# Kernel optimization log

Hardware: AMD Instinct MI355X
Metric: run time of the kernel (lower is better)

## Reference

```python
import jax, jax.numpy as jnp
import numpy as np

B, K, F, E = 32, 1024, 128, 128  # batch, window_size(num_nodes), n_features, embed_dim
OUT2 = 125                       # lin2 output dim (hardcoded in module)
ALPHA = 0.2                      # LeakyReLU negative slope


def setup_inputs() -> dict:
    key = jax.random.key(0)
    ks = jax.random.split(key, 7)
    x = jax.random.normal(ks[0], (B, K, F), dtype=jnp.float32)
    lin_w = jax.random.normal(ks[1], (E, F), dtype=jnp.float32) * 0.05
    lin_b = jax.random.normal(ks[2], (E,), dtype=jnp.float32) * 0.01
    a = jax.random.normal(ks[3], (2 * E, 1), dtype=jnp.float32) * 0.1  # xavier-ish
    bias = jax.random.normal(ks[4], (K, K), dtype=jnp.float32) * 0.02
    lin2_w = jax.random.normal(ks[5], (OUT2, K), dtype=jnp.float32) * 0.03
    lin2_b = jax.random.normal(ks[6], (OUT2,), dtype=jnp.float32) * 0.01
    return {"x": x, "lin_w": lin_w, "lin_b": lin_b, "a": a, "bias": bias,
            "lin2_w": lin2_w, "lin2_b": lin2_b}


def reference(x, lin_w, lin_b, a, bias, lin2_w, lin2_b):
    # Wx = lin(x): [B,K,E]
    Wx = jnp.einsum('bkf,ef->bke', x, lin_w) + lin_b
    # Additive attention scores. Original concatenates (Wx_i, Wx_j) -> [B,K,K,2E]
    # then matmuls with a [2E,1]. Identity: concat @ a == Wx_i@a1 + Wx_j@a2.
    a1 = a[:E, 0]   # [E]
    a2 = a[E:, 0]   # [E]
    s1 = Wx @ a1    # [B,K]  (row/query term, from repeat_interleave)
    s2 = Wx @ a2    # [B,K]  (col/key term, from repeat)
    e = jax.nn.leaky_relu(s1[:, :, None] + s2[:, None, :], negative_slope=ALPHA)
    e = e + bias                              # [B,K,K]
    attention = jax.nn.softmax(e, axis=2)     # softmax over last dim (keys)
    h = jnp.einsum('bij,bjf->bif', attention, x) + x   # [B,K,F], residual
    # permute(0,2,1) -> [B,F,K]; lin2 contracts K -> 125
    h2 = jnp.einsum('bkf,ok->bfo', h, lin2_w) + lin2_b  # [B,F,125]
    h2 = jax.nn.relu(h2)
    return (h2, attention)
```

## Files before the change

### kernel.cpp

```cpp
#include <hip/hip_runtime.h>

#define B_ 32
#define K_ 1024
#define F_ 128
#define E_ 128
#define OUT2_ 125
#define ALPHA_ 0.2f

typedef __bf16 bf16x8_t __attribute__((ext_vector_type(8)));
typedef float  f32x4_t  __attribute__((ext_vector_type(4)));

__device__ __forceinline__ unsigned short f2bf(float f) {
    unsigned u = __float_as_uint(f);
    u = (u + 0x7fffu + ((u >> 16) & 1u)) >> 16;
    return (unsigned short)u;
}

__global__ void k_prep(const float* __restrict__ lin_w, const float* __restrict__ lin_b,
                       const float* __restrict__ a, float* __restrict__ ws) {
    int t = threadIdx.x;
    if (t < 128) {
        float acc = 0.f;
        for (int e = 0; e < E_; ++e) acc += lin_w[e * F_ + t] * a[e];
        ws[t] = acc;
    } else {
        int f = t - 128;
        float acc = 0.f;
        for (int e = 0; e < E_; ++e) acc += lin_w[e * F_ + f] * a[E_ + e];
        ws[128 + f] = acc;
    }
    if (t == 0) { float c = 0.f; for (int e = 0; e < E_; ++e) c += lin_b[e] * a[e];       ws[256] = c; }
    if (t == 1) { float c = 0.f; for (int e = 0; e < E_; ++e) c += lin_b[e] * a[E_ + e];  ws[257] = c; }
}

__global__ __launch_bounds__(256) void k_scores(const float* __restrict__ x,
                                                const float* __restrict__ ws,
                                                float* __restrict__ s1, float* __restrict__ s2) {
    int wave = threadIdx.x >> 6;
    int lane = threadIdx.x & 63;
    int row = blockIdx.x * 4 + wave;
    const float* xr = x + (size_t)row * F_;
    float x0 = xr[lane], x1 = xr[lane + 64];
    float p1 = x0 * ws[lane]       + x1 * ws[lane + 64];
    float p2 = x0 * ws[128 + lane] + x1 * ws[192 + lane];
    for (int m = 32; m; m >>= 1) { p1 += __shfl_xor(p1, m, 64); p2 += __shfl_xor(p2, m, 64); }
    if (lane == 0) { s1[row] = p1 + ws[256]; s2[row] = p2 + ws[257]; }
}

__global__ __launch_bounds__(256) void k_xt(const float* __restrict__ x,
                                            unsigned short* __restrict__ xt) {
    int kt = blockIdx.x;
    int b  = blockIdx.y;
    int t  = threadIdx.x;
    __shared__ float xs[64 * 132];
    const float* xb = x + ((size_t)b * K_ + kt * 64) * F_;
#pragma unroll
    for (int q = 0; q < 8; ++q) {
        int flat = q * 256 + t;
        int kk = flat >> 5, f4 = flat & 31;
        float4 v = *(const float4*)(xb + (size_t)kk * F_ + f4 * 4);
        xs[kk * 132 + f4 * 4]     = v.x;
        xs[kk * 132 + f4 * 4 + 1] = v.y;
        xs[kk * 132 + f4 * 4 + 2] = v.z;
        xs[kk * 132 + f4 * 4 + 3] = v.w;
    }
    __syncthreads();
    int f = t >> 1, half = t & 1;
    union { unsigned short u[32]; uint4 v[4]; } pack;
#pragma unroll
    for (int i = 0; i < 32; ++i) pack.u[i] = f2bf(xs[(half * 32 + i) * 132 + f]);
    unsigned short* dst = xt + (((size_t)(b * 16 + kt) * 128 + f) * 64 + half * 32);
    uint4* d4 = (uint4*)dst;
#pragma unroll
    for (int i = 0; i < 4; ++i) d4[i] = pack.v[i];
}

__global__ __launch_bounds__(256) void k_softmax(const float* __restrict__ s1,
                                                 const float* __restrict__ s2,
                                                 const float* __restrict__ bias,
                                                 float* __restrict__ att) {
    int i = blockIdx.x >> 5;
    int b = blockIdx.x & 31;
    int t = threadIdx.x;
    float sv = s1[b * K_ + i];
    float4 s2v = ((const float4*)(s2 + b * K_))[t];
    float4 bv  = ((const float4*)(bias + (size_t)i * K_))[t];
    float e[4];
    {
        float v;
        v = sv + s2v.x; v = v > 0.f ? v : ALPHA_ * v; e[0] = __expf(v + bv.x);
        v = sv + s2v.y; v = v > 0.f ? v : ALPHA_ * v; e[1] = __expf(v + bv.y);
        v = sv + s2v.z; v = v > 0.f ? v : ALPHA_ * v; e[2] = __expf(v + bv.z);
        v = sv + s2v.w; v = v > 0.f ? v : ALPHA_ * v; e[3] = __expf(v + bv.w);
    }
    float sum = e[0] + e[1] + e[2] + e[3];
    for (int m = 32; m; m >>= 1) sum += __shfl_xor(sum, m, 64);
    __shared__ float reds[4];
    int wave = t >> 6, lane = t & 63;
    if (lane == 0) reds[wave] = sum;
    __syncthreads();
    sum = reds[0] + reds[1] + reds[2] + reds[3];
    float r = 1.f / sum;
    float4 o; o.x = e[0] * r; o.y = e[1] * r; o.z = e[2] * r; o.w = e[3] * r;
    ((float4*)(att + ((size_t)b * K_ + i) * K_))[t] = o;
}

__global__ __launch_bounds__(256) void k_attx(const float* __restrict__ att,
                                              const unsigned short* __restrict__ xt,
                                              const float* __restrict__ x,
                                              unsigned short* __restrict__ h) {
    int b  = blockIdx.y;
    int i0 = blockIdx.x * 64;
    int t  = threadIdx.x;
    int wave = t >> 6, lane = t & 63;
    int quad = lane >> 4, l15 = lane & 15;

    __shared__ unsigned short A_s[64 * 72];
    __shared__ unsigned short X_s[128 * 72];

    const float* ab = att + ((size_t)b * K_ + i0) * K_;

    f32x4_t acc[4][2];
#pragma unroll
    for (int m = 0; m < 4; ++m)
#pragma unroll
        for (int n = 0; n < 2; ++n) acc[m][n] = (f32x4_t)(0.f);

    int ai = t >> 2, aq = t & 3;
    int xf = t >> 1, xh = t & 1;

    for (int kt = 0; kt < 16; ++kt) {
        int k0 = kt * 64;
        __syncthreads();
        {
            const float* src = ab + (size_t)ai * K_ + k0 + aq * 16;
            union { unsigned short u[16]; uint4 v[2]; } p;
#pragma unroll
            for (int q = 0; q < 4; ++q) {
                float4 v = *(const float4*)(src + q * 4);
                p.u[q * 4]     = f2bf(v.x);
                p.u[q * 4 + 1] = f2bf(v.y);
                p.u[q * 4 + 2] = f2bf(v.z);
                p.u[q * 4 + 3] = f2bf(v.w);
            }
            uint4* d = (uint4*)&A_s[ai * 72 + aq * 16];
            d[0] = p.v[0]; d[1] = p.v[1];
        }
        {
            const uint4* src = (const uint4*)(xt + ((size_t)(b * 16 + kt)) * 128 * 64) + t * 4;
            uint4* d = (uint4*)&X_s[xf * 72 + xh * 32];
#pragma unroll
            for (int q = 0; q < 4; ++q) d[q] = src[q];
        }
        __syncthreads();
#pragma unroll
        for (int kh = 0; kh < 2; ++kh) {
            bf16x8_t af[4], bff[2];
#pragma unroll
            for (int m = 0; m < 4; ++m)
                af[m] = *(const bf16x8_t*)&A_s[(m * 16 + l15) * 72 + kh * 32 + quad * 8];
#pragma unroll
            for (int n = 0; n < 2; ++n)
                bff[n] = *(const bf16x8_t*)&X_s[(wave * 32 + n * 16 + l15) * 72 + kh * 32 + quad * 8];
#pragma unroll
            for (int m = 0; m < 4; ++m)
#pragma unroll
                for (int n = 0; n < 2; ++n)
                    acc[m][n] = __builtin_amdgcn_mfma_f32_16x16x32_bf16(af[m], bff[n], acc[m][n], 0, 0, 0);
        }
    }
#pragma unroll
    for (int m = 0; m < 4; ++m) {
#pragma unroll
        for (int n = 0; n < 2; ++n) {
            int f = wave * 32 + n * 16 + l15;
#pragma unroll
            for (int r = 0; r < 4; ++r) {
                int i = i0 + m * 16 + quad * 4 + r;
                size_t idx = ((size_t)b * K_ + i) * F_ + f;
                h[idx] = f2bf(acc[m][n][r] + x[idx]);
            }
        }
    }
}

__global__ __launch_bounds__(256) void k_out2p(const unsigned short* __restrict__ h,
                                               const float* __restrict__ w2,
                                               float* __restrict__ part) {
    int b  = blockIdx.y;
    int f0 = blockIdx.x * 16;
    int ks = blockIdx.z;
    int t = threadIdx.x;
    int o = t & 127;
    int g = t >> 7;
    __shared__ float hs[32 * 24];
    __shared__ float wt[128 * 33];
    const unsigned short* hb = h + (size_t)b * K_ * F_;
    float acc[8];
#pragma unroll
    for (int r = 0; r < 8; ++r) acc[r] = 0.f;

    int kbeg = ks * 256, kend = kbeg + 256;
    for (int k0 = kbeg; k0 < kend; k0 += 32) {
        {
            int idx = t * 2;
            int kk = idx >> 4, ff = idx & 15;
            unsigned pair = *(const unsigned*)(hb + (size_t)(k0 + kk) * F_ + f0 + ff);
            hs[kk * 24 + ff]     = __uint_as_float((pair & 0xFFFFu) << 16);
            hs[kk * 24 + ff + 1] = __uint_as_float((pair >> 16) << 16);
        }
#pragma unroll
        for (int q = 0; q < 16; ++q) {
            int idx = q * 256 + t;
            int oo = idx >> 5, kk = idx & 31;
            wt[oo * 33 + kk] = (oo < OUT2_) ? w2[(size_t)oo * K_ + k0 + kk] : 0.f;
        }
        __syncthreads();
#pragma unroll 8
        for (int kk = 0; kk < 32; ++kk) {
            float4 h0 = *(const float4*)&hs[kk * 24 + g * 8];
            float4 h1 = *(const float4*)&hs[kk * 24 + g * 8 + 4];
            float wv = wt[o * 33 + kk];
            acc[0] += h0.x * wv; acc[1] += h0.y * wv;
            acc[2] += h0.z * wv; acc[3] += h0.w * wv;
            acc[4] += h1.x * wv; acc[5] += h1.y * wv;
            acc[6] += h1.z * wv; acc[7] += h1.w * wv;
        }
        __syncthreads();
    }
#pragma unroll
    for (int r = 0; r < 8; ++r) {
        int f = f0 + g * 8 + r;
        part[((size_t)(ks * 32 + b) * 128 + f) * 128 + o] = acc[r];
    }
}

__global__ __launch_bounds__(256) void k_out2e(const float* __restrict__ part,
                                               const float* __restrict__ b2,
                                               float* __restrict__ out) {
    int idx = blockIdx.x * 256 + threadIdx.x;
    if (idx >= B_ * F_ * OUT2_) return;
    int o  = idx % OUT2_;
    int bf = idx / OUT2_;
    float v = b2[o];
#pragma unroll
    for (int s = 0; s < 4; ++s) v += part[((size_t)s * 4096 + bf) * 128 + o];
    out[idx] = v > 0.f ? v : 0.f;
}

extern "C" void kernel_launch(void* const* d_in, const int* in_sizes, int n_in,
                              void* d_out, int out_size, void* d_ws, size_t ws_size,
                              hipStream_t stream) {
    const float* x      = (const float*)d_in[0];
    const float* lin_w  = (const float*)d_in[1];
    const float* lin_b  = (const float*)d_in[2];
    const float* a      = (const float*)d_in[3];
    const float* bias   = (const float*)d_in[4];
    const float* lin2_w = (const float*)d_in[5];
    const float* lin2_b = (const float*)d_in[6];

    float* out = (float*)d_out;
    float* h2  = out;
    float* att = out + (size_t)B_ * F_ * OUT2_;

    float* ws = (float*)d_ws;
    float* s1 = ws + 512;
    float* s2 = ws + 512 + B_ * K_;
    unsigned short* h  = (unsigned short*)(ws + 512 + 2 * B_ * K_);
    unsigned short* xt = h + (size_t)B_ * K_ * F_;
    float* part = (float*)xt;

    k_prep<<<1, 256, 0, stream>>>(lin_w, lin_b, a, ws);
    k_scores<<<(B_ * K_) / 4, 256, 0, stream>>>(x, ws, s1, s2);
    k_xt<<<dim3(16, B_), 256, 0, stream>>>(x, xt);
    k_softmax<<<B_ * K_, 256, 0, stream>>>(s1, s2, bias, att);
    k_attx<<<dim3(K_ / 64, B_), 256, 0, stream>>>(att, xt, x, h);
    k_out2p<<<dim3(F_ / 16, B_, 4), 256, 0, stream>>>(h, lin2_w, part);
    k_out2e<<<(B_ * F_ * OUT2_ + 255) / 256, 256, 0, stream>>>(part, lin2_b, h2);
}
```

Before: 308.6 us.

## Fuse softmax into attention-times-x kernel, recomputing exps instead of rereading attention

The separate softmax kernel is removed. The attention GEMM kernel now first computes each row's exp-sum from s1, s2 and bias. It then recomputes the normalized probabilities inside the K loop, writes them to the output with nontemporal stores, and feeds them as bf16 to the MFMA. This drops the 128MB round trip of reading attention back from memory. In exchange, every exp is computed twice, and the GEMM kernel takes on extra ALU work and bias reads.

```diff
diff --git a/kernel.cpp b/kernel.cpp
--- a/kernel.cpp
+++ b/kernel.cpp
@@ -75,39 +75,12 @@
     for (int i = 0; i < 4; ++i) d4[i] = pack.v[i];
 }
 
-__global__ __launch_bounds__(256) void k_softmax(const float* __restrict__ s1,
-                                                 const float* __restrict__ s2,
-                                                 const float* __restrict__ bias,
-                                                 float* __restrict__ att) {
-    int i = blockIdx.x >> 5;
-    int b = blockIdx.x & 31;
-    int t = threadIdx.x;
-    float sv = s1[b * K_ + i];
-    float4 s2v = ((const float4*)(s2 + b * K_))[t];
-    float4 bv  = ((const float4*)(bias + (size_t)i * K_))[t];
-    float e[4];
-    {
-        float v;
-        v = sv + s2v.x; v = v > 0.f ? v : ALPHA_ * v; e[0] = __expf(v + bv.x);
-        v = sv + s2v.y; v = v > 0.f ? v : ALPHA_ * v; e[1] = __expf(v + bv.y);
-        v = sv + s2v.z; v = v > 0.f ? v : ALPHA_ * v; e[2] = __expf(v + bv.z);
-        v = sv + s2v.w; v = v > 0.f ? v : ALPHA_ * v; e[3] = __expf(v + bv.w);
-    }
-    float sum = e[0] + e[1] + e[2] + e[3];
-    for (int m = 32; m; m >>= 1) sum += __shfl_xor(sum, m, 64);
-    __shared__ float reds[4];
-    int wave = t >> 6, lane = t & 63;
-    if (lane == 0) reds[wave] = sum;
-    __syncthreads();
-    sum = reds[0] + reds[1] + reds[2] + reds[3];
-    float r = 1.f / sum;
-    float4 o; o.x = e[0] * r; o.y = e[1] * r; o.z = e[2] * r; o.w = e[3] * r;
-    ((float4*)(att + ((size_t)b * K_ + i) * K_))[t] = o;
-}
-
-__global__ __launch_bounds__(256) void k_attx(const float* __restrict__ att,
+__global__ __launch_bounds__(256) void k_attx(const float* __restrict__ s1,
+                                              const float* __restrict__ s2,
+                                              const float* __restrict__ bias,
                                               const unsigned short* __restrict__ xt,
                                               const float* __restrict__ x,
+                                              float* __restrict__ att,
                                               unsigned short* __restrict__ h) {
     int b  = blockIdx.y;
     int i0 = blockIdx.x * 64;
@@ -117,8 +90,27 @@
 
     __shared__ unsigned short A_s[64 * 72];
     __shared__ unsigned short X_s[128 * 72];
-
-    const float* ab = att + ((size_t)b * K_ + i0) * K_;
+    __shared__ float rvs[64];
+
+    int ai = t >> 2, aq = t & 3;
+    float sv = s1[b * K_ + i0 + ai];
+
+    const float4* s2r = (const float4*)(s2 + (size_t)b * K_);
+    const float4* br  = (const float4*)(bias + (size_t)(i0 + ai) * K_);
+    float sum = 0.f;
+#pragma unroll 4
+    for (int q = 0; q < 64; ++q) {
+        float4 s2v = s2r[q * 4 + aq];
+        float4 bv  = br[q * 4 + aq];
+        float v;
+        v = sv + s2v.x; v = v > 0.f ? v : ALPHA_ * v; sum += __expf(v + bv.x);
+        v = sv + s2v.y; v = v > 0.f ? v : ALPHA_ * v; sum += __expf(v + bv.y);
+        v = sv + s2v.z; v = v > 0.f ? v : ALPHA_ * v; sum += __expf(v + bv.z);
+        v = sv + s2v.w; v = v > 0.f ? v : ALPHA_ * v; sum += __expf(v + bv.w);
+    }
+    sum += __shfl_xor(sum, 1, 64);
+    sum += __shfl_xor(sum, 2, 64);
+    if (aq == 0) rvs[ai] = 1.f / sum;
 
     f32x4_t acc[4][2];
 #pragma unroll
@@ -126,22 +118,33 @@
 #pragma unroll
         for (int n = 0; n < 2; ++n) acc[m][n] = (f32x4_t)(0.f);
 
-    int ai = t >> 2, aq = t & 3;
     int xf = t >> 1, xh = t & 1;
 
     for (int kt = 0; kt < 16; ++kt) {
         int k0 = kt * 64;
         __syncthreads();
         {
-            const float* src = ab + (size_t)ai * K_ + k0 + aq * 16;
+            int kb = k0 + aq * 16;
+            float rv = rvs[ai];
+            const float4* s2p = (const float4*)(s2 + (size_t)b * K_ + kb);
+            const float4* bp  = (const float4*)(bias + (size_t)(i0 + ai) * K_ + kb);
+            f32x4_t* ap = (f32x4_t*)(att + ((size_t)b * K_ + i0 + ai) * K_ + kb);
             union { unsigned short u[16]; uint4 v[2]; } p;
 #pragma unroll
             for (int q = 0; q < 4; ++q) {
-                float4 v = *(const float4*)(src + q * 4);
-                p.u[q * 4]     = f2bf(v.x);
-                p.u[q * 4 + 1] = f2bf(v.y);
-                p.u[q * 4 + 2] = f2bf(v.z);
-                p.u[q * 4 + 3] = f2bf(v.w);
+                float4 s2v = s2p[q];
+                float4 bv  = bp[q];
+                f32x4_t e;
+                float v;
+                v = sv + s2v.x; v = v > 0.f ? v : ALPHA_ * v; e[0] = __expf(v + bv.x) * rv;
+                v = sv + s2v.y; v = v > 0.f ? v : ALPHA_ * v; e[1] = __expf(v + bv.y) * rv;
+                v = sv + s2v.z; v = v > 0.f ? v : ALPHA_ * v; e[2] = __expf(v + bv.z) * rv;
+                v = sv + s2v.w; v = v > 0.f ? v : ALPHA_ * v; e[3] = __expf(v + bv.w) * rv;
+                __builtin_nontemporal_store(e, ap + q);
+                p.u[q * 4]     = f2bf(e[0]);
+                p.u[q * 4 + 1] = f2bf(e[1]);
+                p.u[q * 4 + 2] = f2bf(e[2]);
+                p.u[q * 4 + 3] = f2bf(e[3]);
             }
             uint4* d = (uint4*)&A_s[ai * 72 + aq * 16];
             d[0] = p.v[0]; d[1] = p.v[1];
@@ -273,8 +276,7 @@
     k_prep<<<1, 256, 0, stream>>>(lin_w, lin_b, a, ws);
     k_scores<<<(B_ * K_) / 4, 256, 0, stream>>>(x, ws, s1, s2);
     k_xt<<<dim3(16, B_), 256, 0, stream>>>(x, xt);
-    k_softmax<<<B_ * K_, 256, 0, stream>>>(s1, s2, bias, att);
-    k_attx<<<dim3(K_ / 64, B_), 256, 0, stream>>>(att, xt, x, h);
+    k_attx<<<dim3(K_ / 64, B_), 256, 0, stream>>>(s1, s2, bias, xt, x, att, h);
     k_out2p<<<dim3(F_ / 16, B_, 4), 256, 0, stream>>>(h, lin2_w, part);
     k_out2e<<<(B_ * F_ * OUT2_ + 255) / 256, 256, 0, stream>>>(part, lin2_b, h2);
 }
```

Result: slower. 478.2 us (+55.0%).

## Recompute attention probabilities in attx from scores instead of reading att

Applied to the files above, without the earlier changes.

The attention-times-x kernel no longer reads the 128MB fp32 attention matrix written by the softmax kernel. It rebuilds each softmax row from s1, s2 and bias, first with a row-sum pass and then by recomputing the exponentials per tile. This removes a large read of HBM traffic in exchange for extra exp work and a second read of the bias rows, which are small and shared across batches and so likely cache-resident. The softmax kernel still writes att because it is an output.

```diff
diff --git a/kernel.cpp b/kernel.cpp
--- a/kernel.cpp
+++ b/kernel.cpp
@@ -105,7 +105,9 @@
     ((float4*)(att + ((size_t)b * K_ + i) * K_))[t] = o;
 }
 
-__global__ __launch_bounds__(256) void k_attx(const float* __restrict__ att,
+__global__ __launch_bounds__(256) void k_attx(const float* __restrict__ s1,
+                                              const float* __restrict__ s2,
+                                              const float* __restrict__ bias,
                                               const unsigned short* __restrict__ xt,
                                               const float* __restrict__ x,
                                               unsigned short* __restrict__ h) {
@@ -117,8 +119,29 @@
 
     __shared__ unsigned short A_s[64 * 72];
     __shared__ unsigned short X_s[128 * 72];
-
-    const float* ab = att + ((size_t)b * K_ + i0) * K_;
+    __shared__ float rvs[64];
+
+    int ai = t >> 2, aq = t & 3;
+    float sv = s1[b * K_ + i0 + ai];
+
+    const float4* s2r = (const float4*)(s2 + (size_t)b * K_);
+    const float4* br  = (const float4*)(bias + (size_t)(i0 + ai) * K_);
+    float sum = 0.f;
+#pragma unroll 4
+    for (int q = 0; q < 64; ++q) {
+        float4 s2v = s2r[q * 4 + aq];
+        float4 bv  = br[q * 4 + aq];
+        float v;
+        v = sv + s2v.x; v = v > 0.f ? v : ALPHA_ * v; sum += __expf(v + bv.x);
+        v = sv + s2v.y; v = v > 0.f ? v : ALPHA_ * v; sum += __expf(v + bv.y);
+        v = sv + s2v.z; v = v > 0.f ? v : ALPHA_ * v; sum += __expf(v + bv.z);
+        v = sv + s2v.w; v = v > 0.f ? v : ALPHA_ * v; sum += __expf(v + bv.w);
+    }
+    sum += __shfl_xor(sum, 1, 64);
+    sum += __shfl_xor(sum, 2, 64);
+    if (aq == 0) rvs[ai] = 1.f / sum;
+    __syncthreads();
+    float rv = rvs[ai];
 
     f32x4_t acc[4][2];
 #pragma unroll
@@ -126,22 +149,25 @@
 #pragma unroll
         for (int n = 0; n < 2; ++n) acc[m][n] = (f32x4_t)(0.f);
 
-    int ai = t >> 2, aq = t & 3;
     int xf = t >> 1, xh = t & 1;
 
     for (int kt = 0; kt < 16; ++kt) {
         int k0 = kt * 64;
         __syncthreads();
         {
-            const float* src = ab + (size_t)ai * K_ + k0 + aq * 16;
+            int kb = k0 + aq * 16;
+            const float4* s2p = (const float4*)(s2 + (size_t)b * K_ + kb);
+            const float4* bp  = (const float4*)(bias + (size_t)(i0 + ai) * K_ + kb);
             union { unsigned short u[16]; uint4 v[2]; } p;
 #pragma unroll
             for (int q = 0; q < 4; ++q) {
-                float4 v = *(const float4*)(src + q * 4);
-                p.u[q * 4]     = f2bf(v.x);
-                p.u[q * 4 + 1] = f2bf(v.y);
-                p.u[q * 4 + 2] = f2bf(v.z);
-                p.u[q * 4 + 3] = f2bf(v.w);
+                float4 s2v = s2p[q];
+                float4 bv  = bp[q];
+                float v, e;
+                v = sv + s2v.x; v = v > 0.f ? v : ALPHA_ * v; e = __expf(v + bv.x) * rv; p.u[q * 4]     = f2bf(e);
+                v = sv + s2v.y; v = v > 0.f ? v : ALPHA_ * v; e = __expf(v + bv.y) * rv; p.u[q * 4 + 1] = f2bf(e);
+                v = sv + s2v.z; v = v > 0.f ? v : ALPHA_ * v; e = __expf(v + bv.z) * rv; p.u[q * 4 + 2] = f2bf(e);
+                v = sv + s2v.w; v = v > 0.f ? v : ALPHA_ * v; e = __expf(v + bv.w) * rv; p.u[q * 4 + 3] = f2bf(e);
             }
             uint4* d = (uint4*)&A_s[ai * 72 + aq * 16];
             d[0] = p.v[0]; d[1] = p.v[1];
@@ -274,7 +300,7 @@
     k_scores<<<(B_ * K_) / 4, 256, 0, stream>>>(x, ws, s1, s2);
     k_xt<<<dim3(16, B_), 256, 0, stream>>>(x, xt);
     k_softmax<<<B_ * K_, 256, 0, stream>>>(s1, s2, bias, att);
-    k_attx<<<dim3(K_ / 64, B_), 256, 0, stream>>>(att, xt, x, h);
+    k_attx<<<dim3(K_ / 64, B_), 256, 0, stream>>>(s1, s2, bias, xt, x, h);
     k_out2p<<<dim3(F_ / 16, B_, 4), 256, 0, stream>>>(h, lin2_w, part);
     k_out2e<<<(B_ * F_ * OUT2_ + 255) / 256, 256, 0, stream>>>(part, lin2_b, h2);
 }
```

Measured after the change: 330.7 us. +7.1%, slower.

## Use MFMA for lin2 with transposed h and halve attx row tile

Applied to the files above, without the earlier changes.

The attention-times-x kernel now writes h transposed ([B,F,K]) and uses 32-row tiles, doubling its grid. The scalar FP32 lin2 split-K kernel and its reduction kernel are replaced by one bf16 MFMA kernel that converts lin2_w to bf16 in shared memory and fuses bias and ReLU. This removes the partial-sum buffer, one launch and the scalar FMA loop. The cost is lower precision for lin2 weights, only 64 blocks in the new kernel, and lin2_w re-converted by every block.

```diff
diff --git a/kernel.cpp b/kernel.cpp
--- a/kernel.cpp
+++ b/kernel.cpp
@@ -108,43 +108,38 @@
 __global__ __launch_bounds__(256) void k_attx(const float* __restrict__ att,
                                               const unsigned short* __restrict__ xt,
                                               const float* __restrict__ x,
-                                              unsigned short* __restrict__ h) {
+                                              unsigned short* __restrict__ ht) {
     int b  = blockIdx.y;
-    int i0 = blockIdx.x * 64;
+    int i0 = blockIdx.x * 32;
     int t  = threadIdx.x;
     int wave = t >> 6, lane = t & 63;
     int quad = lane >> 4, l15 = lane & 15;
 
-    __shared__ unsigned short A_s[64 * 72];
+    __shared__ unsigned short A_s[32 * 72];
     __shared__ unsigned short X_s[128 * 72];
 
     const float* ab = att + ((size_t)b * K_ + i0) * K_;
 
-    f32x4_t acc[4][2];
-#pragma unroll
-    for (int m = 0; m < 4; ++m)
+    f32x4_t acc[2][2];
+#pragma unroll
+    for (int m = 0; m < 2; ++m)
 #pragma unroll
         for (int n = 0; n < 2; ++n) acc[m][n] = (f32x4_t)(0.f);
 
-    int ai = t >> 2, aq = t & 3;
+    int ai = t >> 3, aq = t & 7;
     int xf = t >> 1, xh = t & 1;
 
     for (int kt = 0; kt < 16; ++kt) {
         int k0 = kt * 64;
         __syncthreads();
         {
-            const float* src = ab + (size_t)ai * K_ + k0 + aq * 16;
-            union { unsigned short u[16]; uint4 v[2]; } p;
-#pragma unroll
-            for (int q = 0; q < 4; ++q) {
-                float4 v = *(const float4*)(src + q * 4);
-                p.u[q * 4]     = f2bf(v.x);
-                p.u[q * 4 + 1] = f2bf(v.y);
-                p.u[q * 4 + 2] = f2bf(v.z);
-                p.u[q * 4 + 3] = f2bf(v.w);
-            }
-            uint4* d = (uint4*)&A_s[ai * 72 + aq * 16];
-            d[0] = p.v[0]; d[1] = p.v[1];
+            const float* src = ab + (size_t)ai * K_ + k0 + aq * 8;
+            float4 v0 = *(const float4*)(src);
+            float4 v1 = *(const float4*)(src + 4);
+            union { unsigned short u[8]; uint4 v; } p;
+            p.u[0] = f2bf(v0.x); p.u[1] = f2bf(v0.y); p.u[2] = f2bf(v0.z); p.u[3] = f2bf(v0.w);
+            p.u[4] = f2bf(v1.x); p.u[5] = f2bf(v1.y); p.u[6] = f2bf(v1.z); p.u[7] = f2bf(v1.w);
+            *(uint4*)&A_s[ai * 72 + aq * 8] = p.v;
         }
         {
             const uint4* src = (const uint4*)(xt + ((size_t)(b * 16 + kt)) * 128 * 64) + t * 4;
@@ -155,97 +150,110 @@
         __syncthreads();
 #pragma unroll
         for (int kh = 0; kh < 2; ++kh) {
-            bf16x8_t af[4], bff[2];
-#pragma unroll
-            for (int m = 0; m < 4; ++m)
+            bf16x8_t af[2], bff[2];
+#pragma unroll
+            for (int m = 0; m < 2; ++m)
                 af[m] = *(const bf16x8_t*)&A_s[(m * 16 + l15) * 72 + kh * 32 + quad * 8];
 #pragma unroll
             for (int n = 0; n < 2; ++n)
                 bff[n] = *(const bf16x8_t*)&X_s[(wave * 32 + n * 16 + l15) * 72 + kh * 32 + quad * 8];
 #pragma unroll
-            for (int m = 0; m < 4; ++m)
+            for (int m = 0; m < 2; ++m)
 #pragma unroll
                 for (int n = 0; n < 2; ++n)
                     acc[m][n] = __builtin_amdgcn_mfma_f32_16x16x32_bf16(af[m], bff[n], acc[m][n], 0, 0, 0);
         }
     }
 #pragma unroll
-    for (int m = 0; m < 4; ++m) {
+    for (int m = 0; m < 2; ++m) {
 #pragma unroll
         for (int n = 0; n < 2; ++n) {
             int f = wave * 32 + n * 16 + l15;
+            int ib = i0 + m * 16 + quad * 4;
+            union { unsigned short u[4]; ushort4 v; } p;
 #pragma unroll
             for (int r = 0; r < 4; ++r) {
-                int i = i0 + m * 16 + quad * 4 + r;
-                size_t idx = ((size_t)b * K_ + i) * F_ + f;
-                h[idx] = f2bf(acc[m][n][r] + x[idx]);
-            }
-        }
-    }
-}
-
-__global__ __launch_bounds__(256) void k_out2p(const unsigned short* __restrict__ h,
+                int i = ib + r;
+                p.u[r] = f2bf(acc[m][n][r] + x[((size_t)b * K_ + i) * F_ + f]);
+            }
+            *(ushort4*)&ht[((size_t)b * F_ + f) * K_ + ib] = p.v;
+        }
+    }
+}
+
+__global__ __launch_bounds__(256) void k_out2m(const unsigned short* __restrict__ ht,
                                                const float* __restrict__ w2,
-                                               float* __restrict__ part) {
-    int b  = blockIdx.y;
-    int f0 = blockIdx.x * 16;
-    int ks = blockIdx.z;
-    int t = threadIdx.x;
-    int o = t & 127;
-    int g = t >> 7;
-    __shared__ float hs[32 * 24];
-    __shared__ float wt[128 * 33];
-    const unsigned short* hb = h + (size_t)b * K_ * F_;
-    float acc[8];
-#pragma unroll
-    for (int r = 0; r < 8; ++r) acc[r] = 0.f;
-
-    int kbeg = ks * 256, kend = kbeg + 256;
-    for (int k0 = kbeg; k0 < kend; k0 += 32) {
-        {
-            int idx = t * 2;
-            int kk = idx >> 4, ff = idx & 15;
-            unsigned pair = *(const unsigned*)(hb + (size_t)(k0 + kk) * F_ + f0 + ff);
-            hs[kk * 24 + ff]     = __uint_as_float((pair & 0xFFFFu) << 16);
-            hs[kk * 24 + ff + 1] = __uint_as_float((pair >> 16) << 16);
-        }
-#pragma unroll
-        for (int q = 0; q < 16; ++q) {
-            int idx = q * 256 + t;
-            int oo = idx >> 5, kk = idx & 31;
-            wt[oo * 33 + kk] = (oo < OUT2_) ? w2[(size_t)oo * K_ + k0 + kk] : 0.f;
-        }
-        __syncthreads();
-#pragma unroll 8
-        for (int kk = 0; kk < 32; ++kk) {
-            float4 h0 = *(const float4*)&hs[kk * 24 + g * 8];
-            float4 h1 = *(const float4*)&hs[kk * 24 + g * 8 + 4];
-            float wv = wt[o * 33 + kk];
-            acc[0] += h0.x * wv; acc[1] += h0.y * wv;
-            acc[2] += h0.z * wv; acc[3] += h0.w * wv;
-            acc[4] += h1.x * wv; acc[5] += h1.y * wv;
-            acc[6] += h1.z * wv; acc[7] += h1.w * wv;
-        }
-        __syncthreads();
-    }
-#pragma unroll
-    for (int r = 0; r < 8; ++r) {
-        int f = f0 + g * 8 + r;
-        part[((size_t)(ks * 32 + b) * 128 + f) * 128 + o] = acc[r];
-    }
-}
-
-__global__ __launch_bounds__(256) void k_out2e(const float* __restrict__ part,
                                                const float* __restrict__ b2,
                                                float* __restrict__ out) {
-    int idx = blockIdx.x * 256 + threadIdx.x;
-    if (idx >= B_ * F_ * OUT2_) return;
-    int o  = idx % OUT2_;
-    int bf = idx / OUT2_;
-    float v = b2[o];
-#pragma unroll
-    for (int s = 0; s < 4; ++s) v += part[((size_t)s * 4096 + bf) * 128 + o];
-    out[idx] = v > 0.f ? v : 0.f;
+    int b  = blockIdx.y;
+    int f0 = blockIdx.x * 64;
+    int t  = threadIdx.x;
+    int wave = t >> 6, lane = t & 63;
+    int quad = lane >> 4, l15 = lane & 15;
+
+    __shared__ unsigned short W_s[128 * 72];
+    __shared__ unsigned short H_s[64 * 72];
+
+    f32x4_t acc[8];
+#pragma unroll
+    for (int m = 0; m < 8; ++m) acc[m] = (f32x4_t)(0.f);
+
+    int wo = t >> 1, wq = t & 1;
+    int hf = t >> 2, hq = t & 3;
+
+    for (int kt = 0; kt < 16; ++kt) {
+        int k0 = kt * 64;
+        __syncthreads();
+        {
+            union { unsigned short u[32]; uint4 v[4]; } p;
+            if (wo < OUT2_) {
+                const float* src = w2 + (size_t)wo * K_ + k0 + wq * 32;
+#pragma unroll
+                for (int q = 0; q < 8; ++q) {
+                    float4 v = *(const float4*)(src + q * 4);
+                    p.u[q * 4]     = f2bf(v.x);
+                    p.u[q * 4 + 1] = f2bf(v.y);
+                    p.u[q * 4 + 2] = f2bf(v.z);
+                    p.u[q * 4 + 3] = f2bf(v.w);
+                }
+            } else {
+#pragma unroll
+                for (int q = 0; q < 4; ++q) p.v[q] = make_uint4(0, 0, 0, 0);
+            }
+            uint4* d = (uint4*)&W_s[wo * 72 + wq * 32];
+#pragma unroll
+            for (int q = 0; q < 4; ++q) d[q] = p.v[q];
+        }
+        {
+            const uint4* src = (const uint4*)(ht + ((size_t)b * F_ + f0 + hf) * K_ + k0) + hq * 2;
+            uint4* d = (uint4*)&H_s[hf * 72 + hq * 16];
+            d[0] = src[0]; d[1] = src[1];
+        }
+        __syncthreads();
+#pragma unroll
+        for (int kh = 0; kh < 2; ++kh) {
+            bf16x8_t bf = *(const bf16x8_t*)&H_s[(wave * 16 + l15) * 72 + kh * 32 + quad * 8];
+#pragma unroll
+            for (int m = 0; m < 8; ++m) {
+                bf16x8_t af = *(const bf16x8_t*)&W_s[(m * 16 + l15) * 72 + kh * 32 + quad * 8];
+                acc[m] = __builtin_amdgcn_mfma_f32_16x16x32_bf16(af, bf, acc[m], 0, 0, 0);
+            }
+        }
+    }
+    int f = f0 + wave * 16 + l15;
+    float* orow = out + ((size_t)b * F_ + f) * OUT2_;
+#pragma unroll
+    for (int m = 0; m < 8; ++m) {
+        int ob = m * 16 + quad * 4;
+#pragma unroll
+        for (int r = 0; r < 4; ++r) {
+            int o = ob + r;
+            if (o < OUT2_) {
+                float v = acc[m][r] + b2[o];
+                orow[o] = v > 0.f ? v : 0.f;
+            }
+        }
+    }
 }
 
 extern "C" void kernel_launch(void* const* d_in, const int* in_sizes, int n_in,
@@ -266,15 +274,13 @@
     float* ws = (float*)d_ws;
     float* s1 = ws + 512;
     float* s2 = ws + 512 + B_ * K_;
-    unsigned short* h  = (unsigned short*)(ws + 512 + 2 * B_ * K_);
-    unsigned short* xt = h + (size_t)B_ * K_ * F_;
-    float* part = (float*)xt;
+    unsigned short* ht = (unsigned short*)(ws + 512 + 2 * B_ * K_);
+    unsigned short* xt = ht + (size_t)B_ * K_ * F_;
 
     k_prep<<<1, 256, 0, stream>>>(lin_w, lin_b, a, ws);
     k_scores<<<(B_ * K_) / 4, 256, 0, stream>>>(x, ws, s1, s2);
     k_xt<<<dim3(16, B_), 256, 0, stream>>>(x, xt);
     k_softmax<<<B_ * K_, 256, 0, stream>>>(s1, s2, bias, att);
-    k_attx<<<dim3(K_ / 64, B_), 256, 0, stream>>>(att, xt, x, h);
-    k_out2p<<<dim3(F_ / 16, B_, 4), 256, 0, stream>>>(h, lin2_w, part);
-    k_out2e<<<(B_ * F_ * OUT2_ + 255) / 256, 256, 0, stream>>>(part, lin2_b, h2);
-}
+    k_attx<<<dim3(K_ / 32, B_), 256, 0, stream>>>(att, xt, x, ht);
+    k_out2m<<<dim3(2, B_), 256, 0, stream>>>(ht, lin2_w, lin2_b, h2);
+}
```

Result: faster. 293.8 us (-4.8%).
